# Performance work log

Hardware: AMD Instinct MI355X
Metric: run time of the kernel (lower is better)

## Reference

```python
import jax, jax.numpy as jnp
import numpy as np

E, C, N, W_IN, W_OUT = 5, 2, 2048, 512, 256


def setup_inputs() -> dict:
    key = jax.random.key(0)
    ks = jax.random.split(key, 11)
    A = jax.random.uniform(ks[0], (E, N, N), dtype=jnp.float32)  # stacked edge-type adjacencies
    X = jax.random.normal(ks[1], (N, W_IN), dtype=jnp.float32)
    # GTConv weights (out_channels=C, in_channels=E), init std=0.01 as in torch
    gt_w0a = 0.01 * jax.random.normal(ks[2], (C, E), dtype=jnp.float32)
    gt_w0b = 0.01 * jax.random.normal(ks[3], (C, E), dtype=jnp.float32)
    gt_w1 = 0.01 * jax.random.normal(ks[4], (C, E), dtype=jnp.float32)
    gcn_w = jax.random.normal(ks[5], (W_IN, W_OUT), dtype=jnp.float32) / np.sqrt(W_IN)
    gcn_b = jnp.zeros((W_OUT,), dtype=jnp.float32)
    lin1_w = 0.02 * jax.random.normal(ks[6], (W_OUT, C * W_OUT), dtype=jnp.float32)
    lin1_b = jnp.zeros((W_OUT,), dtype=jnp.float32)
    lin2_w = 0.02 * jax.random.normal(ks[7], (W_OUT, W_OUT), dtype=jnp.float32)
    lin2_b = jnp.zeros((W_OUT,), dtype=jnp.float32)
    return {"A": A, "X": X, "gt_w0a": gt_w0a, "gt_w0b": gt_w0b, "gt_w1": gt_w1,
            "gcn_w": gcn_w, "gcn_b": gcn_b, "lin1_w": lin1_w, "lin1_b": lin1_b,
            "lin2_w": lin2_w, "lin2_b": lin2_b}


def _gtconv(w, A):
    # softmax over edge types, weighted sum of adjacencies == coalesce of scaled edge lists
    f = jax.nn.softmax(w, axis=1)  # (C, E)
    return jnp.einsum('ce,enm->cnm', f, A)  # (C, N, N)


def _normalize(H):
    # remove self loops, then divide each entry by its column (target) degree
    n = H.shape[-1]
    H = H * (1.0 - jnp.eye(n, dtype=H.dtype))
    deg = H.sum(axis=-2)                      # (C, N) column sums == scatter_add over col
    safe = jnp.where(deg != 0, deg, 1.0)
    dinv = jnp.where(deg != 0, 1.0 / safe, 0.0)
    return H * dinv[:, None, :]


def reference(A, X, gt_w0a, gt_w0b, gt_w1, gcn_w, gcn_b, lin1_w, lin1_b, lin2_w, lin2_b):
    # layer 0 (first=True): two GTConvs, per-channel spspmm == batched matmul
    Ha = _gtconv(gt_w0a, A)
    Hb = _gtconv(gt_w0b, A)
    H = _normalize(jnp.einsum('cij,cjk->cik', Ha, Hb))
    # layer 1 (first=False): H_ @ conv1(A)
    Hb2 = _gtconv(gt_w1, A)
    H = _normalize(jnp.einsum('cij,cjk->cik', H, Hb2))
    # GCNConv per channel: add self loops, symmetric deg^{-1/2} normalization, aggregate to col
    n = H.shape[-1]
    M = H + jnp.eye(n, dtype=H.dtype)         # (C, N, N)
    deg = M.sum(axis=-2)                      # (C, N)
    safe = jnp.where(deg > 0, deg, 1.0)
    dis = jnp.where(deg > 0, safe ** -0.5, 0.0)
    Ahat = dis[:, :, None] * M * dis[:, None, :]
    XW = X @ gcn_w                            # (N, W_OUT)
    out = jnp.einsum('crn,rf->cnf', Ahat, XW) + gcn_b  # out[c,n] = sum_r Ahat[c,r,n] XW[r]
    out = jax.nn.relu(out)                    # (C, N, W_OUT)
    Xcat = out.transpose(1, 0, 2).reshape(n, -1)       # concat channels along dim=1
    h = jax.nn.relu(Xcat @ lin1_w.T + lin1_b)
    return h @ lin2_w.T + lin2_b
```

## Files before the change

kernel.cpp:

```cpp
#include <hip/hip_runtime.h>
#include <cstdint>
#include <cstddef>

#define NN   2048
#define N2   (2048LL*2048LL)
#define CC   2
#define EE   5
#define WIN  512
#define WOUT 256

typedef __bf16 bf16_t;
typedef __attribute__((ext_vector_type(8))) __bf16 bf16x8;
typedef __attribute__((ext_vector_type(4))) __bf16 bf16x4;
typedef __attribute__((ext_vector_type(4))) float  f32x4;

__global__ void k_prep(const float* __restrict__ X, const float* __restrict__ l1w,
                       const float* __restrict__ l2w, const float* __restrict__ gcnw,
                       bf16_t* __restrict__ Xb, bf16_t* __restrict__ l1wb,
                       bf16_t* __restrict__ l2wb, bf16_t* __restrict__ gwT) {
  __shared__ bf16_t tile[64][65];
  int bid = blockIdx.x;
  if (bid < 608) {
    int i = bid * 256 + threadIdx.x;
    const float* src; bf16_t* dst; int off;
    if (i < 131072)      { src = X;   dst = Xb;   off = i; }
    else if (i < 147456) { src = l1w; dst = l1wb; off = i - 131072; }
    else if (i < 155648) { src = l2w; dst = l2wb; off = i - 147456; }
    else return;
    float4 a = ((const float4*)src)[off * 2];
    float4 b = ((const float4*)src)[off * 2 + 1];
    bf16x8 o;
    o[0] = (bf16_t)a.x; o[1] = (bf16_t)a.y; o[2] = (bf16_t)a.z; o[3] = (bf16_t)a.w;
    o[4] = (bf16_t)b.x; o[5] = (bf16_t)b.y; o[6] = (bf16_t)b.z; o[7] = (bf16_t)b.w;
    ((bf16x8*)dst)[off] = o;
  } else {
    int b2 = bid - 608;
    int m0 = (b2 & 7) * 64, n0 = (b2 >> 3) * 64;
    int t = threadIdx.x, tr = t >> 4, tc = (t & 15) << 2;
#pragma unroll
    for (int v = 0; v < 4; ++v) {
      int r = tr + v * 16;
      float4 d = *(const float4*)&gcnw[(long long)(m0 + r) * WOUT + n0 + tc];
      tile[r][tc + 0] = (bf16_t)d.x; tile[r][tc + 1] = (bf16_t)d.y;
      tile[r][tc + 2] = (bf16_t)d.z; tile[r][tc + 3] = (bf16_t)d.w;
    }
    __syncthreads();
#pragma unroll
    for (int v = 0; v < 4; ++v) {
      int r = tr + v * 16;
      bf16x4 o;
      o[0] = tile[tc + 0][r]; o[1] = tile[tc + 1][r];
      o[2] = tile[tc + 2][r]; o[3] = tile[tc + 3][r];
      *(bf16x4*)&gwT[(long long)(n0 + r) * WIN + m0 + tc] = o;
    }
  }
}


__global__ void k_combine(const float* __restrict__ A,
                          const float* __restrict__ w0a, const float* __restrict__ w0b,
                          const float* __restrict__ w1,
                          bf16_t* __restrict__ Ha, bf16_t* __restrict__ HbT,
                          bf16_t* __restrict__ Hb2T, float* __restrict__ part) {
  __shared__ bf16_t tl[2][64][65];
  __shared__ float cs[2][16][64];
  float f[3][2][5];
  {
    const float* wp[3] = {w0a, w0b, w1};
#pragma unroll
    for (int w = 0; w < 3; ++w)
#pragma unroll
      for (int c = 0; c < 2; ++c) {
        float x[5], m = -1e30f, s = 0.f;
#pragma unroll
        for (int e = 0; e < 5; ++e) { x[e] = wp[w][c * 5 + e]; m = fmaxf(m, x[e]); }
#pragma unroll
        for (int e = 0; e < 5; ++e) { x[e] = expf(x[e] - m); s += x[e]; }
#pragma unroll
        for (int e = 0; e < 5; ++e) f[w][c][e] = x[e] / s;
      }
  }
  int i0 = blockIdx.x * 64, j0 = blockIdx.y * 64;
  int t = threadIdx.x, tr = t >> 4, tc = (t & 15) << 2;
  float cs0[4] = {0, 0, 0, 0}, cs1[4] = {0, 0, 0, 0};
  bf16x4 hb2a[4], hb2b[4];

#pragma unroll
  for (int v = 0; v < 4; ++v) {
    int lr = tr + v * 16;
    long long gi = i0 + lr;
    const float* base = A + gi * (long long)NN + j0 + tc;
    float av[5][4];
#pragma unroll
    for (int e = 0; e < 5; ++e) {
      float4 q = *(const float4*)(base + (long long)e * N2);
      av[e][0] = q.x; av[e][1] = q.y; av[e][2] = q.z; av[e][3] = q.w;
    }
    bf16x4 ha0, ha1;
#pragma unroll
    for (int x = 0; x < 4; ++x) {
      float s0 = 0.f, s1 = 0.f, s2 = 0.f, s3 = 0.f, s4 = 0.f, s5 = 0.f;
#pragma unroll
      for (int e = 0; e < 5; ++e) {
        float u = av[e][x];
        s0 += f[0][0][e] * u; s1 += f[0][1][e] * u;
        s2 += f[1][0][e] * u; s3 += f[1][1][e] * u;
        s4 += f[2][0][e] * u; s5 += f[2][1][e] * u;
      }
      ha0[x] = (bf16_t)s0; cs0[x] += (float)ha0[x];
      ha1[x] = (bf16_t)s1; cs1[x] += (float)ha1[x];
      tl[0][lr][tc + x] = (bf16_t)s2; tl[1][lr][tc + x] = (bf16_t)s3;
      hb2a[v][x] = (bf16_t)s4; hb2b[v][x] = (bf16_t)s5;
    }
    *(bf16x4*)&Ha[0 * N2 + gi * NN + j0 + tc] = ha0;
    *(bf16x4*)&Ha[1 * N2 + gi * NN + j0 + tc] = ha1;
  }
#pragma unroll
  for (int x = 0; x < 4; ++x) { cs[0][tr][tc + x] = cs0[x]; cs[1][tr][tc + x] = cs1[x]; }
  __syncthreads();

#pragma unroll
  for (int v = 0; v < 4; ++v) {
    int lr = tr + v * 16;
#pragma unroll
    for (int ch = 0; ch < 2; ++ch) {
      bf16x4 o;
      o[0] = tl[ch][tc + 0][lr]; o[1] = tl[ch][tc + 1][lr];
      o[2] = tl[ch][tc + 2][lr]; o[3] = tl[ch][tc + 3][lr];
      *(bf16x4*)&HbT[(long long)ch * N2 + (long long)(j0 + lr) * NN + i0 + tc] = o;
    }
  }
  if (t < 128) {
    int ch = t >> 6, col = t & 63;
    float s = 0.f;
#pragma unroll
    for (int r = 0; r < 16; ++r) s += cs[ch][r][col];
    part[((long long)ch * 32 + blockIdx.x) * NN + j0 + col] = s;
  }
  __syncthreads();

#pragma unroll
  for (int v = 0; v < 4; ++v) {
    int lr = tr + v * 16;
#pragma unroll
    for (int x = 0; x < 4; ++x) {
      tl[0][lr][tc + x] = hb2a[v][x];
      tl[1][lr][tc + x] = hb2b[v][x];
    }
  }
  __syncthreads();

#pragma unroll
  for (int v = 0; v < 4; ++v) {
    int lr = tr + v * 16;
#pragma unroll
    for (int ch = 0; ch < 2; ++ch) {
      bf16x4 o;
      o[0] = tl[ch][tc + 0][lr]; o[1] = tl[ch][tc + 1][lr];
      o[2] = tl[ch][tc + 2][lr]; o[3] = tl[ch][tc + 3][lr];
      *(bf16x4*)&Hb2T[(long long)ch * N2 + (long long)(j0 + lr) * NN + i0 + tc] = o;
    }
  }
}

__global__ void k_s_finish(const float* __restrict__ part, float* __restrict__ s) {
  int idx = blockIdx.x * 256 + threadIdx.x;
  int c = idx >> 11, k = idx & 2047;
  float acc = 0.f;
#pragma unroll
  for (int ib = 0; ib < 32; ++ib) acc += part[((long long)c * 32 + ib) * NN + k];
  s[idx] = acc;
}

template<bool EMIT_DIS>
__global__ void k_deg(const float* __restrict__ svec, const bf16_t* __restrict__ Arows,
                      const bf16_t* __restrict__ BT,
                      float* __restrict__ out1, float* __restrict__ out2,
                      float* __restrict__ out3) {
  int c = blockIdx.y;
  int j = blockIdx.x * 4 + (threadIdx.x >> 6);
  int lane = threadIdx.x & 63;
  const bf16_t* a = Arows + (long long)c * N2 + (long long)j * NN;
  const bf16_t* b = BT + (long long)c * N2 + (long long)j * NN;
  const float* s = svec + c * NN;
  float acc_s = 0.f, acc_a = 0.f;
#pragma unroll
  for (int it = 0; it < 4; ++it) {
    int k0 = (lane + it * 64) * 8;
    bf16x8 av = *(const bf16x8*)(a + k0);
    bf16x8 bv = *(const bf16x8*)(b + k0);
    float4 s0 = *(const float4*)(s + k0);
    float4 s1 = *(const float4*)(s + k0 + 4);
    float sv[8] = {s0.x, s0.y, s0.z, s0.w, s1.x, s1.y, s1.z, s1.w};
#pragma unroll
    for (int x = 0; x < 8; ++x) {
      float bx = (float)bv[x];
      acc_s += sv[x] * bx;
      acc_a += (float)av[x] * bx;
    }
  }
#pragma unroll
  for (int o = 32; o > 0; o >>= 1) {
    acc_s += __shfl_xor(acc_s, o, 64);
    acc_a += __shfl_xor(acc_a, o, 64);
  }
  if (lane == 0) {
    float deg = acc_s - acc_a;
    bool nz = (deg != 0.f);
    if (!EMIT_DIS) {
      out1[c * NN + j] = nz ? 1.f / deg : 0.f;
      out2[c * NN + j] = nz ? 1.f : 0.f;
    } else {
      float dis = nz ? 0.70710678118654752f : 1.f;
      out1[c * NN + j] = nz ? dis / deg : 0.f;
      out2[c * NN + j] = dis;
      out3[c * NN + j] = acc_a;
    }
  }
}

__global__ void k_scale_xwd(const bf16_t* __restrict__ XWT, const float* __restrict__ disv,
                            bf16_t* __restrict__ XWdT) {
  int i = blockIdx.x * 256 + threadIdx.x;
  int c = i >> 16, rem = i & 65535;
  bf16x8 v = ((const bf16x8*)XWT)[rem];
  int col0 = (rem & 255) * 8;
  float4 d0 = *(const float4*)(disv + c * NN + col0);
  float4 d1 = *(const float4*)(disv + c * NN + col0 + 4);
  bf16x8 o;
  o[0] = (bf16_t)((float)v[0] * d0.x); o[1] = (bf16_t)((float)v[1] * d0.y);
  o[2] = (bf16_t)((float)v[2] * d0.z); o[3] = (bf16_t)((float)v[3] * d0.w);
  o[4] = (bf16_t)((float)v[4] * d1.x); o[5] = (bf16_t)((float)v[5] * d1.y);
  o[6] = (bf16_t)((float)v[6] * d1.z); o[7] = (bf16_t)((float)v[7] * d1.w);
  ((bf16x8*)XWdT)[i] = o;
}


__global__ __launch_bounds__(256)
void k_gemmL(const bf16_t* __restrict__ A, const bf16_t* __restrict__ B,
             bf16_t* __restrict__ Hn, bf16_t* __restrict__ HnT,
             const float* __restrict__ dinv) {
  __shared__ __align__(16) char smem[65536];
  bf16_t* As = (bf16_t*)smem;
  bf16_t* Bs = (bf16_t*)(smem + 32768);
  bf16_t* tile = (bf16_t*)smem;

  int cz = blockIdx.z;
  const bf16_t* Ab = A + cz * N2 + (long long)blockIdx.x * 128 * NN;
  const bf16_t* Bb = B + cz * N2 + (long long)blockIdx.y * 128 * NN;

  int t = threadIdx.x, wid = t >> 6, lane = t & 63;
  int wr = wid >> 1, wc = wid & 1;
  f32x4 acc[4][4] = {};
  int frow = lane & 15;
  int fk_sw = (((lane >> 4) ^ ((frow >> 1) & 3)) << 3);
  int srow = t >> 2;
  int scol_sw = (((t & 3) ^ ((t >> 3) & 3)) << 3);

  auto STAGE = [&](int TT, int BUF) {
#pragma unroll
    for (int s = 0; s < 2; ++s) {
      long long kko = (long long)TT * 64 + s * 32 + scol_sw;
      const bf16_t* ga0 = Ab + (long long)srow * NN + kko;
      const bf16_t* gb0 = Bb + (long long)srow * NN + kko;
      char* la = smem + BUF * 16384 + s * 8192 + wid * 1024;
      char* lb = smem + 32768 + BUF * 16384 + s * 8192 + wid * 1024;
      __builtin_amdgcn_global_load_lds((__attribute__((address_space(1))) void*)ga0,
          (__attribute__((address_space(3))) void*)la, 16, 0, 0);
      __builtin_amdgcn_global_load_lds((__attribute__((address_space(1))) void*)(ga0 + 64LL * NN),
          (__attribute__((address_space(3))) void*)(la + 4096), 16, 0, 0);
      __builtin_amdgcn_global_load_lds((__attribute__((address_space(1))) void*)gb0,
          (__attribute__((address_space(3))) void*)lb, 16, 0, 0);
      __builtin_amdgcn_global_load_lds((__attribute__((address_space(1))) void*)(gb0 + 64LL * NN),
          (__attribute__((address_space(3))) void*)(lb + 4096), 16, 0, 0);
    }
  };
  auto COMPUTE = [&](int BUF) {
#pragma unroll
    for (int ks = 0; ks < 2; ++ks) {
      bf16x8 af[4], bfr[4];
#pragma unroll
      for (int m = 0; m < 4; ++m)
        af[m] = *(const bf16x8*)&As[BUF * 8192 + ks * 4096 + (wr * 64 + m * 16 + frow) * 32 + fk_sw];
#pragma unroll
      for (int n = 0; n < 4; ++n)
        bfr[n] = *(const bf16x8*)&Bs[BUF * 8192 + ks * 4096 + (wc * 64 + n * 16 + frow) * 32 + fk_sw];
      __builtin_amdgcn_s_setprio(1);
#pragma unroll
      for (int m = 0; m < 4; ++m)
#pragma unroll
        for (int n = 0; n < 4; ++n)
          acc[m][n] = __builtin_amdgcn_mfma_f32_16x16x32_bf16(af[m], bfr[n], acc[m][n], 0, 0, 0);
      __builtin_amdgcn_s_setprio(0);
    }
  };

  const int nt = 32;
  STAGE(0, 0); STAGE(1, 1);
  for (int tt = 0; tt < nt; ++tt) {
    if (tt < nt - 1) asm volatile("s_waitcnt vmcnt(8)" ::: "memory");
    else             asm volatile("s_waitcnt vmcnt(0)" ::: "memory");
    __builtin_amdgcn_s_barrier();
    __builtin_amdgcn_sched_barrier(0);
    COMPUTE(tt & 1);
    __builtin_amdgcn_s_barrier();
    if (tt + 2 < nt) STAGE(tt + 2, tt & 1);
  }
  __builtin_amdgcn_sched_barrier(0);

  int rl0 = wr * 64 + ((lane >> 4) << 2);
  int cl0 = wc * 64 + (lane & 15);
  int r0 = blockIdx.x * 128 + rl0;
  int c0 = blockIdx.y * 128 + cl0;

  bf16_t* Cb = Hn + cz * N2;
  bf16_t* Ct = HnT + cz * N2;
  float dj[4];
#pragma unroll
  for (int n = 0; n < 4; ++n) dj[n] = dinv[cz * NN + c0 + n * 16];
#pragma unroll
  for (int m = 0; m < 4; ++m)
#pragma unroll
    for (int n = 0; n < 4; ++n)
#pragma unroll
      for (int j = 0; j < 4; ++j) {
        int r = r0 + m * 16 + j, col = c0 + n * 16;
        float v = (r == col) ? 0.f : acc[m][n][j] * dj[n];
        Cb[(long long)r * NN + col] = (bf16_t)v;
        tile[(rl0 + m * 16 + j) * 130 + cl0 + n * 16] = (bf16_t)v;
      }
  __syncthreads();
  int nl = t >> 5, rl = (t & 31) * 4;
#pragma unroll
  for (int vv = 0; vv < 16; ++vv) {
    int n_l = nl + vv * 8;
    bf16x4 o;
    o[0] = tile[(rl + 0) * 130 + n_l]; o[1] = tile[(rl + 1) * 130 + n_l];
    o[2] = tile[(rl + 2) * 130 + n_l]; o[3] = tile[(rl + 3) * 130 + n_l];
    *(bf16x4*)&Ct[(long long)(blockIdx.y * 128 + n_l) * NN + blockIdx.x * 128 + rl] = o;
  }
}


enum { EP_F32 = 0, EP_BRELU = 3, EP_BF32 = 4, EP_XWT = 5, EP_BF16O = 7 };

template<int EP>
__global__ __launch_bounds__(256)
void k_gemm(const bf16_t* __restrict__ A, const bf16_t* __restrict__ B,
            void* __restrict__ Cv,
            const float* __restrict__ aux1, const float* __restrict__ aux2,
            bf16_t* __restrict__ aux3,
            int N, int K, int lda, int ldb,
            long long zA, long long zB, long long zC) {
  __shared__ __align__(16) char smem[36864];
  bf16_t* As = (bf16_t*)smem;
  bf16_t* Bs = (bf16_t*)(smem + 24576);
  bf16_t* tile = (bf16_t*)smem;

  int cz = blockIdx.z;
  const bf16_t* Ab = A + cz * zA + (long long)blockIdx.x * 128 * lda;
  const bf16_t* Bb = B + cz * zB + (long long)blockIdx.y * 64 * ldb;

  int t = threadIdx.x, wid = t >> 6, lane = t & 63;
  int wr = wid >> 1, wc = wid & 1;
  f32x4 acc[4][2] = {};
  int frow = lane & 15;
  int fk_sw = (((lane >> 4) ^ ((frow >> 1) & 3)) << 3);
  int srow = t >> 2;
  int scol_sw = (((t & 3) ^ ((t >> 3) & 3)) << 3);
  int nt = K >> 5;

  auto STAGE = [&](int TT, int BUF) {
    long long kko = (long long)TT * 32 + scol_sw;
    const bf16_t* ga0 = Ab + (long long)srow * lda + kko;
    const bf16_t* ga1 = Ab + (long long)(64 + srow) * lda + kko;
    const bf16_t* gb0 = Bb + (long long)srow * ldb + kko;
    char* la = smem + BUF * 8192 + wid * 1024;
    char* lb = smem + 24576 + BUF * 4096 + wid * 1024;
    __builtin_amdgcn_global_load_lds((__attribute__((address_space(1))) void*)ga0,
        (__attribute__((address_space(3))) void*)la, 16, 0, 0);
    __builtin_amdgcn_global_load_lds((__attribute__((address_space(1))) void*)ga1,
        (__attribute__((address_space(3))) void*)(la + 4096), 16, 0, 0);
    __builtin_amdgcn_global_load_lds((__attribute__((address_space(1))) void*)gb0,
        (__attribute__((address_space(3))) void*)lb, 16, 0, 0);
  };
  auto COMPUTE = [&](int BUF) {
    bf16x8 af[4], bfr[2];
#pragma unroll
    for (int m = 0; m < 4; ++m)
      af[m] = *(const bf16x8*)&As[BUF * 4096 + (wr * 64 + m * 16 + frow) * 32 + fk_sw];
#pragma unroll
    for (int n = 0; n < 2; ++n)
      bfr[n] = *(const bf16x8*)&Bs[BUF * 2048 + (wc * 32 + n * 16 + frow) * 32 + fk_sw];
#pragma unroll
    for (int m = 0; m < 4; ++m)
#pragma unroll
      for (int n = 0; n < 2; ++n)
        acc[m][n] = __builtin_amdgcn_mfma_f32_16x16x32_bf16(af[m], bfr[n], acc[m][n], 0, 0, 0);
  };

  STAGE(0, 0); STAGE(1, 1); STAGE(2, 2);
  int slot = 0;
  for (int tt = 0; tt < nt; ++tt) {
    int rem = nt - 1 - tt;
    if (rem >= 2)      asm volatile("s_waitcnt vmcnt(6)" ::: "memory");
    else if (rem == 1) asm volatile("s_waitcnt vmcnt(3)" ::: "memory");
    else               asm volatile("s_waitcnt vmcnt(0)" ::: "memory");
    __builtin_amdgcn_s_barrier();
    __builtin_amdgcn_sched_barrier(0);
    COMPUTE(slot);
    __builtin_amdgcn_s_barrier();
    if (tt + 3 < nt) STAGE(tt + 3, slot);
    slot = (slot == 2) ? 0 : slot + 1;
  }
  __builtin_amdgcn_sched_barrier(0);

  int rl0 = wr * 64 + ((lane >> 4) << 2);
  int cl0 = wc * 32 + (lane & 15);
  int r0 = blockIdx.x * 128 + rl0;
  int c0 = blockIdx.y * 64 + cl0;

  if constexpr (EP == EP_F32) {
    float* Cb = (float*)Cv + cz * zC;
#pragma unroll
    for (int m = 0; m < 4; ++m)
#pragma unroll
      for (int n = 0; n < 2; ++n)
#pragma unroll
        for (int j = 0; j < 4; ++j)
          Cb[(long long)(r0 + m * 16 + j) * N + c0 + n * 16] = acc[m][n][j];
  } else if constexpr (EP == EP_BF16O) {
    bf16_t* Cb = (bf16_t*)Cv + cz * zC;
#pragma unroll
    for (int m = 0; m < 4; ++m)
#pragma unroll
      for (int n = 0; n < 2; ++n)
#pragma unroll
        for (int j = 0; j < 4; ++j)
          Cb[(long long)(r0 + m * 16 + j) * N + c0 + n * 16] = (bf16_t)acc[m][n][j];
  } else if constexpr (EP == EP_XWT) {
    float* Cb = (float*)Cv;
#pragma unroll
    for (int m = 0; m < 4; ++m)
#pragma unroll
      for (int n = 0; n < 2; ++n)
#pragma unroll
        for (int j = 0; j < 4; ++j) {
          float v = acc[m][n][j];
          Cb[(long long)(r0 + m * 16 + j) * N + c0 + n * 16] = v;
          tile[(rl0 + m * 16 + j) * 65 + cl0 + n * 16] = (bf16_t)v;
        }
    __syncthreads();
    int nl = t >> 5, rl = (t & 31) * 4;
#pragma unroll
    for (int vv = 0; vv < 8; ++vv) {
      int n_l = nl + vv * 8;
      bf16x4 o;
      o[0] = tile[(rl + 0) * 65 + n_l]; o[1] = tile[(rl + 1) * 65 + n_l];
      o[2] = tile[(rl + 2) * 65 + n_l]; o[3] = tile[(rl + 3) * 65 + n_l];
      *(bf16x4*)&aux3[(long long)(blockIdx.y * 64 + n_l) * NN + blockIdx.x * 128 + rl] = o;
    }
  } else if constexpr (EP == EP_BRELU) {
    bf16_t* Cb = (bf16_t*)Cv;
    float bj[2];
#pragma unroll
    for (int n = 0; n < 2; ++n) bj[n] = aux1[c0 + n * 16];
#pragma unroll
    for (int m = 0; m < 4; ++m)
#pragma unroll
      for (int n = 0; n < 2; ++n)
#pragma unroll
        for (int j = 0; j < 4; ++j)
          Cb[(long long)(r0 + m * 16 + j) * N + c0 + n * 16] =
              (bf16_t)fmaxf(acc[m][n][j] + bj[n], 0.f);
  } else {
    float* Cb = (float*)Cv;
    float bj[2];
#pragma unroll
    for (int n = 0; n < 2; ++n) bj[n] = aux1[c0 + n * 16];
#pragma unroll
    for (int m = 0; m < 4; ++m)
#pragma unroll
      for (int n = 0; n < 2; ++n)
#pragma unroll
        for (int j = 0; j < 4; ++j)
          Cb[(long long)(r0 + m * 16 + j) * N + c0 + n * 16] = acc[m][n][j] + bj[n];
  }
}


__global__ void k_gcn_epi2(const float* __restrict__ Z, const float* __restrict__ XW,
                           const float* __restrict__ gcn_b, const float* __restrict__ cscal,
                           const float* __restrict__ disv, const float* __restrict__ Mdiag,
                           bf16_t* __restrict__ Xcat) {
  long long idx4 = ((long long)blockIdx.x * 256 + threadIdx.x) * 4;
  int c = (int)(idx4 >> 19);
  int rem = (int)(idx4 & ((1 << 19) - 1));
  int n = rem >> 8, fcol = rem & 255;
  float4 z  = *(const float4*)(Z + (long long)c * NN * WOUT + rem);
  float4 xw = *(const float4*)(XW + rem);
  float4 b  = *(const float4*)(gcn_b + fcol);
  float cs = cscal[c * NN + n], dn = disv[c * NN + n], md = Mdiag[c * NN + n];
  float d2 = dn * dn, mdd = md * dn;
  bf16x4 o;
  o[0] = (bf16_t)fmaxf(cs * (z.x - mdd * xw.x) + d2 * xw.x + b.x, 0.f);
  o[1] = (bf16_t)fmaxf(cs * (z.y - mdd * xw.y) + d2 * xw.y + b.y, 0.f);
  o[2] = (bf16_t)fmaxf(cs * (z.z - mdd * xw.z) + d2 * xw.z + b.z, 0.f);
  o[3] = (bf16_t)fmaxf(cs * (z.w - mdd * xw.w) + d2 * xw.w + b.w, 0.f);
  *(bf16x4*)&Xcat[(long long)n * (CC * WOUT) + c * WOUT + fcol] = o;
}


extern "C" void kernel_launch(void* const* d_in, const int* in_sizes, int n_in,
                              void* d_out, int out_size, void* d_ws, size_t ws_size,
                              hipStream_t stream) {
  const float* A    = (const float*)d_in[0];
  const float* X    = (const float*)d_in[1];
  const float* w0a  = (const float*)d_in[2];
  const float* w0b  = (const float*)d_in[3];
  const float* w1   = (const float*)d_in[4];
  const float* gcnw = (const float*)d_in[5];
  const float* gcnb = (const float*)d_in[6];
  const float* l1w  = (const float*)d_in[7];
  const float* l1b  = (const float*)d_in[8];
  const float* l2w  = (const float*)d_in[9];
  const float* l2b  = (const float*)d_in[10];
  float* out = (float*)d_out;

  char* p = (char*)d_ws;
  auto carve = [&](size_t bytes) -> char* {
    char* r = p; p += (bytes + 255) & ~(size_t)255; return r;
  };
  float*  svec  = (float*)carve((size_t)CC * NN * 4);
  float*  dinv1 = (float*)carve((size_t)CC * NN * 4);
  float*  m1    = (float*)carve((size_t)CC * NN * 4);
  float*  cscal = (float*)carve((size_t)CC * NN * 4);
  float*  disv  = (float*)carve((size_t)CC * NN * 4);
  float*  Mdiag = (float*)carve((size_t)CC * NN * 4);
  float*  part  = (float*)carve((size_t)CC * 32 * NN * 4);
  bf16_t* S1    = (bf16_t*)carve((size_t)CC * N2 * 2);
  bf16_t* HbT   = (bf16_t*)carve((size_t)CC * N2 * 2);
  bf16_t* Hb2T  = (bf16_t*)carve((size_t)CC * N2 * 2);
  bf16_t* Hn    = (bf16_t*)carve((size_t)CC * N2 * 2);
  bf16_t* HnT   = (bf16_t*)carve((size_t)CC * N2 * 2);
  bf16_t* Xb    = (bf16_t*)carve((size_t)NN * WIN * 2);
  bf16_t* gwT   = (bf16_t*)carve((size_t)WOUT * WIN * 2);
  bf16_t* l1wb  = (bf16_t*)carve((size_t)WOUT * CC * WOUT * 2);
  bf16_t* l2wb  = (bf16_t*)carve((size_t)WOUT * WOUT * 2);
  float*  XW    = (float*)carve((size_t)NN * WOUT * 4);
  bf16_t* XWT   = (bf16_t*)carve((size_t)WOUT * NN * 2);
  bf16_t* Xcat  = (bf16_t*)carve((size_t)NN * CC * WOUT * 2);
  bf16_t* hb    = (bf16_t*)carve((size_t)NN * WOUT * 2);

  bf16_t* Ha = S1;
  bf16_t* XWdT = (bf16_t*)((char*)S1);
  bf16_t* Yt   = (bf16_t*)((char*)S1 + (2LL << 20));
  float*  Z    = (float*) ((char*)S1 + (6LL << 20));

  k_prep<<<640, 256, 0, stream>>>(X, l1w, l2w, gcnw, Xb, l1wb, l2wb, gwT);
  k_combine<<<dim3(32, 32), 256, 0, stream>>>(A, w0a, w0b, w1, Ha, HbT, Hb2T, part);
  k_s_finish<<<16, 256, 0, stream>>>(part, svec);

  k_deg<false><<<dim3(512, 2), 256, 0, stream>>>(svec, Ha, HbT, dinv1, m1, nullptr);
  k_gemmL<<<dim3(16, 16, 2), 256, 0, stream>>>(Ha, HbT, Hn, HnT, dinv1);

  k_deg<true><<<dim3(512, 2), 256, 0, stream>>>(m1, Hn, Hb2T, cscal, disv, Mdiag);

  k_gemm<EP_XWT><<<dim3(16, 4, 1), 256, 0, stream>>>(
      Xb, gwT, XW, nullptr, nullptr, XWT, WOUT, WIN, WIN, WIN, 0, 0, 0);
  k_scale_xwd<<<512, 256, 0, stream>>>(XWT, disv, XWdT);
  k_gemm<EP_BF16O><<<dim3(2, 32, 2), 256, 0, stream>>>(
      XWdT, HnT, Yt, nullptr, nullptr, nullptr, NN, NN, NN, NN,
      (long long)WOUT * NN, N2, (long long)WOUT * NN);
  k_gemm<EP_F32><<<dim3(16, 4, 2), 256, 0, stream>>>(
      Hb2T, Yt, Z, nullptr, nullptr, nullptr, WOUT, NN, NN, NN,
      N2, (long long)WOUT * NN, (long long)NN * WOUT);
  k_gcn_epi2<<<1024, 256, 0, stream>>>(Z, XW, gcnb, cscal, disv, Mdiag, Xcat);

  k_gemm<EP_BRELU><<<dim3(16, 4, 1), 256, 0, stream>>>(
      Xcat, l1wb, hb, l1b, nullptr, nullptr, WOUT, CC * WOUT, CC * WOUT, CC * WOUT, 0, 0, 0);
  k_gemm<EP_BF32><<<dim3(16, 4, 1), 256, 0, stream>>>(
      hb, l2wb, out, l2b, nullptr, nullptr, WOUT, WOUT, WOUT, WOUT, 0, 0, 0);
}
```

Before: 149.9 us.

## Fuse prep, scaling and GCN epilogue kernels into neighbouring launches

Merges the weight/X bf16 conversion into the combine kernel as extra blocks, folds the dis-scaling of XW^T into the XW GEMM epilogue, and folds the GCN epilogue into the Z GEMM so Z is never materialized in fp32. The combine column-sum reduction now uses wave shuffles instead of a 16-row shared array. This removes three launches and the round trips through the XWT and Z buffers, at the cost of more complex epilogues with uncoalesced scalar stores and gathers in the GCN epilogue.

```diff
diff --git a/kernel.cpp b/kernel.cpp
--- a/kernel.cpp
+++ b/kernel.cpp
@@ -14,56 +14,63 @@
 typedef __attribute__((ext_vector_type(4))) __bf16 bf16x4;
 typedef __attribute__((ext_vector_type(4))) float  f32x4;
 
-__global__ void k_prep(const float* __restrict__ X, const float* __restrict__ l1w,
-                       const float* __restrict__ l2w, const float* __restrict__ gcnw,
-                       bf16_t* __restrict__ Xb, bf16_t* __restrict__ l1wb,
-                       bf16_t* __restrict__ l2wb, bf16_t* __restrict__ gwT) {
-  __shared__ bf16_t tile[64][65];
-  int bid = blockIdx.x;
-  if (bid < 608) {
-    int i = bid * 256 + threadIdx.x;
-    const float* src; bf16_t* dst; int off;
-    if (i < 131072)      { src = X;   dst = Xb;   off = i; }
-    else if (i < 147456) { src = l1w; dst = l1wb; off = i - 131072; }
-    else if (i < 155648) { src = l2w; dst = l2wb; off = i - 147456; }
-    else return;
-    float4 a = ((const float4*)src)[off * 2];
-    float4 b = ((const float4*)src)[off * 2 + 1];
-    bf16x8 o;
-    o[0] = (bf16_t)a.x; o[1] = (bf16_t)a.y; o[2] = (bf16_t)a.z; o[3] = (bf16_t)a.w;
-    o[4] = (bf16_t)b.x; o[5] = (bf16_t)b.y; o[6] = (bf16_t)b.z; o[7] = (bf16_t)b.w;
-    ((bf16x8*)dst)[off] = o;
-  } else {
-    int b2 = bid - 608;
-    int m0 = (b2 & 7) * 64, n0 = (b2 >> 3) * 64;
-    int t = threadIdx.x, tr = t >> 4, tc = (t & 15) << 2;
-#pragma unroll
-    for (int v = 0; v < 4; ++v) {
-      int r = tr + v * 16;
-      float4 d = *(const float4*)&gcnw[(long long)(m0 + r) * WOUT + n0 + tc];
-      tile[r][tc + 0] = (bf16_t)d.x; tile[r][tc + 1] = (bf16_t)d.y;
-      tile[r][tc + 2] = (bf16_t)d.z; tile[r][tc + 3] = (bf16_t)d.w;
-    }
-    __syncthreads();
-#pragma unroll
-    for (int v = 0; v < 4; ++v) {
-      int r = tr + v * 16;
-      bf16x4 o;
-      o[0] = tile[tc + 0][r]; o[1] = tile[tc + 1][r];
-      o[2] = tile[tc + 2][r]; o[3] = tile[tc + 3][r];
-      *(bf16x4*)&gwT[(long long)(n0 + r) * WIN + m0 + tc] = o;
-    }
-  }
-}
+#define AS1 __attribute__((address_space(1)))
+#define AS3 __attribute__((address_space(3)))
 
 
 __global__ void k_combine(const float* __restrict__ A,
                           const float* __restrict__ w0a, const float* __restrict__ w0b,
                           const float* __restrict__ w1,
                           bf16_t* __restrict__ Ha, bf16_t* __restrict__ HbT,
-                          bf16_t* __restrict__ Hb2T, float* __restrict__ part) {
+                          bf16_t* __restrict__ Hb2T, float* __restrict__ part,
+                          const float* __restrict__ X, const float* __restrict__ l1w,
+                          const float* __restrict__ l2w, const float* __restrict__ gcnw,
+                          bf16_t* __restrict__ Xb, bf16_t* __restrict__ l1wb,
+                          bf16_t* __restrict__ l2wb, bf16_t* __restrict__ gwT) {
   __shared__ bf16_t tl[2][64][65];
-  __shared__ float cs[2][16][64];
+  __shared__ float cs[2][4][64];
+  int bid = blockIdx.x;
+  int t = threadIdx.x;
+
+  if (bid >= 1024) {
+    int bid2 = bid - 1024;
+    if (bid2 < 608) {
+      int i = bid2 * 256 + t;
+      const float* src; bf16_t* dst; int off;
+      if (i < 131072)      { src = X;   dst = Xb;   off = i; }
+      else if (i < 147456) { src = l1w; dst = l1wb; off = i - 131072; }
+      else                 { src = l2w; dst = l2wb; off = i - 147456; }
+      float4 a = ((const float4*)src)[off * 2];
+      float4 b = ((const float4*)src)[off * 2 + 1];
+      bf16x8 o;
+      o[0] = (bf16_t)a.x; o[1] = (bf16_t)a.y; o[2] = (bf16_t)a.z; o[3] = (bf16_t)a.w;
+      o[4] = (bf16_t)b.x; o[5] = (bf16_t)b.y; o[6] = (bf16_t)b.z; o[7] = (bf16_t)b.w;
+      ((bf16x8*)dst)[off] = o;
+    } else {
+      int b2 = bid2 - 608;
+      int m0 = (b2 & 7) * 64, n0 = (b2 >> 3) * 64;
+      int tr = t >> 4, tc = (t & 15) << 2;
+      bf16_t (*tile)[65] = (bf16_t (*)[65])&tl[0][0][0];
+#pragma unroll
+      for (int v = 0; v < 4; ++v) {
+        int r = tr + v * 16;
+        float4 d = *(const float4*)&gcnw[(long long)(m0 + r) * WOUT + n0 + tc];
+        tile[r][tc + 0] = (bf16_t)d.x; tile[r][tc + 1] = (bf16_t)d.y;
+        tile[r][tc + 2] = (bf16_t)d.z; tile[r][tc + 3] = (bf16_t)d.w;
+      }
+      __syncthreads();
+#pragma unroll
+      for (int v = 0; v < 4; ++v) {
+        int r = tr + v * 16;
+        bf16x4 o;
+        o[0] = tile[tc + 0][r]; o[1] = tile[tc + 1][r];
+        o[2] = tile[tc + 2][r]; o[3] = tile[tc + 3][r];
+        *(bf16x4*)&gwT[(long long)(n0 + r) * WIN + m0 + tc] = o;
+      }
+    }
+    return;
+  }
+
   float f[3][2][5];
   {
     const float* wp[3] = {w0a, w0b, w1};
@@ -80,8 +87,9 @@
         for (int e = 0; e < 5; ++e) f[w][c][e] = x[e] / s;
       }
   }
-  int i0 = blockIdx.x * 64, j0 = blockIdx.y * 64;
-  int t = threadIdx.x, tr = t >> 4, tc = (t & 15) << 2;
+  int i0 = (bid >> 5) * 64, j0 = (bid & 31) * 64;
+  int tr = t >> 4, tc = (t & 15) << 2;
+  int lane = t & 63, wid = t >> 6;
   float cs0[4] = {0, 0, 0, 0}, cs1[4] = {0, 0, 0, 0};
   bf16x4 hb2a[4], hb2b[4];
 
@@ -116,7 +124,15 @@
     *(bf16x4*)&Ha[1 * N2 + gi * NN + j0 + tc] = ha1;
   }
 #pragma unroll
-  for (int x = 0; x < 4; ++x) { cs[0][tr][tc + x] = cs0[x]; cs[1][tr][tc + x] = cs1[x]; }
+  for (int x = 0; x < 4; ++x) {
+    float a0 = cs0[x], a1 = cs1[x];
+    a0 += __shfl_xor(a0, 16, 64); a0 += __shfl_xor(a0, 32, 64);
+    a1 += __shfl_xor(a1, 16, 64); a1 += __shfl_xor(a1, 32, 64);
+    if ((lane >> 4) == 0) {
+      cs[0][wid][(lane & 15) * 4 + x] = a0;
+      cs[1][wid][(lane & 15) * 4 + x] = a1;
+    }
+  }
   __syncthreads();
 
 #pragma unroll
@@ -132,10 +148,8 @@
   }
   if (t < 128) {
     int ch = t >> 6, col = t & 63;
-    float s = 0.f;
-#pragma unroll
-    for (int r = 0; r < 16; ++r) s += cs[ch][r][col];
-    part[((long long)ch * 32 + blockIdx.x) * NN + j0 + col] = s;
+    float s = cs[ch][0][col] + cs[ch][1][col] + cs[ch][2][col] + cs[ch][3][col];
+    part[((long long)ch * 32 + (bid >> 5)) * NN + j0 + col] = s;
   }
   __syncthreads();
 
@@ -219,22 +233,6 @@
   }
 }
 
-__global__ void k_scale_xwd(const bf16_t* __restrict__ XWT, const float* __restrict__ disv,
-                            bf16_t* __restrict__ XWdT) {
-  int i = blockIdx.x * 256 + threadIdx.x;
-  int c = i >> 16, rem = i & 65535;
-  bf16x8 v = ((const bf16x8*)XWT)[rem];
-  int col0 = (rem & 255) * 8;
-  float4 d0 = *(const float4*)(disv + c * NN + col0);
-  float4 d1 = *(const float4*)(disv + c * NN + col0 + 4);
-  bf16x8 o;
-  o[0] = (bf16_t)((float)v[0] * d0.x); o[1] = (bf16_t)((float)v[1] * d0.y);
-  o[2] = (bf16_t)((float)v[2] * d0.z); o[3] = (bf16_t)((float)v[3] * d0.w);
-  o[4] = (bf16_t)((float)v[4] * d1.x); o[5] = (bf16_t)((float)v[5] * d1.y);
-  o[6] = (bf16_t)((float)v[6] * d1.z); o[7] = (bf16_t)((float)v[7] * d1.w);
-  ((bf16x8*)XWdT)[i] = o;
-}
-
 
 __global__ __launch_bounds__(256)
 void k_gemmL(const bf16_t* __restrict__ A, const bf16_t* __restrict__ B,
@@ -265,14 +263,10 @@
       const bf16_t* gb0 = Bb + (long long)srow * NN + kko;
       char* la = smem + BUF * 16384 + s * 8192 + wid * 1024;
       char* lb = smem + 32768 + BUF * 16384 + s * 8192 + wid * 1024;
-      __builtin_amdgcn_global_load_lds((__attribute__((address_space(1))) void*)ga0,
-          (__attribute__((address_space(3))) void*)la, 16, 0, 0);
-      __builtin_amdgcn_global_load_lds((__attribute__((address_space(1))) void*)(ga0 + 64LL * NN),
-          (__attribute__((address_space(3))) void*)(la + 4096), 16, 0, 0);
-      __builtin_amdgcn_global_load_lds((__attribute__((address_space(1))) void*)gb0,
-          (__attribute__((address_space(3))) void*)lb, 16, 0, 0);
-      __builtin_amdgcn_global_load_lds((__attribute__((address_space(1))) void*)(gb0 + 64LL * NN),
-          (__attribute__((address_space(3))) void*)(lb + 4096), 16, 0, 0);
+      __builtin_amdgcn_global_load_lds((AS1 void*)ga0, (AS3 void*)la, 16, 0, 0);
+      __builtin_amdgcn_global_load_lds((AS1 void*)(ga0 + 64LL * NN), (AS3 void*)(la + 4096), 16, 0, 0);
+      __builtin_amdgcn_global_load_lds((AS1 void*)gb0, (AS3 void*)lb, 16, 0, 0);
+      __builtin_amdgcn_global_load_lds((AS1 void*)(gb0 + 64LL * NN), (AS3 void*)(lb + 4096), 16, 0, 0);
     }
   };
   auto COMPUTE = [&](int BUF) {
@@ -342,14 +336,14 @@
 }
 
 
-enum { EP_F32 = 0, EP_BRELU = 3, EP_BF32 = 4, EP_XWT = 5, EP_BF16O = 7 };
+enum { EP_BRELU = 3, EP_BF32 = 4, EP_BF16O = 7, EP_XWDT = 8, EP_GCN = 9 };
 
 template<int EP>
 __global__ __launch_bounds__(256)
 void k_gemm(const bf16_t* __restrict__ A, const bf16_t* __restrict__ B,
             void* __restrict__ Cv,
             const float* __restrict__ aux1, const float* __restrict__ aux2,
-            bf16_t* __restrict__ aux3,
+            bf16_t* __restrict__ aux3, const float* __restrict__ aux4,
             int N, int K, int lda, int ldb,
             long long zA, long long zB, long long zC) {
   __shared__ __align__(16) char smem[36864];
@@ -377,12 +371,9 @@
     const bf16_t* gb0 = Bb + (long long)srow * ldb + kko;
     char* la = smem + BUF * 8192 + wid * 1024;
     char* lb = smem + 24576 + BUF * 4096 + wid * 1024;
-    __builtin_amdgcn_global_load_lds((__attribute__((address_space(1))) void*)ga0,
-        (__attribute__((address_space(3))) void*)la, 16, 0, 0);
-    __builtin_amdgcn_global_load_lds((__attribute__((address_space(1))) void*)ga1,
-        (__attribute__((address_space(3))) void*)(la + 4096), 16, 0, 0);
-    __builtin_amdgcn_global_load_lds((__attribute__((address_space(1))) void*)gb0,
-        (__attribute__((address_space(3))) void*)lb, 16, 0, 0);
+    __builtin_amdgcn_global_load_lds((AS1 void*)ga0, (AS3 void*)la, 16, 0, 0);
+    __builtin_amdgcn_global_load_lds((AS1 void*)ga1, (AS3 void*)(la + 4096), 16, 0, 0);
+    __builtin_amdgcn_global_load_lds((AS1 void*)gb0, (AS3 void*)lb, 16, 0, 0);
   };
   auto COMPUTE = [&](int BUF) {
     bf16x8 af[4], bfr[2];
@@ -420,16 +411,7 @@
   int r0 = blockIdx.x * 128 + rl0;
   int c0 = blockIdx.y * 64 + cl0;
 
-  if constexpr (EP == EP_F32) {
-    float* Cb = (float*)Cv + cz * zC;
-#pragma unroll
-    for (int m = 0; m < 4; ++m)
-#pragma unroll
-      for (int n = 0; n < 2; ++n)
-#pragma unroll
-        for (int j = 0; j < 4; ++j)
-          Cb[(long long)(r0 + m * 16 + j) * N + c0 + n * 16] = acc[m][n][j];
-  } else if constexpr (EP == EP_BF16O) {
+  if constexpr (EP == EP_BF16O) {
     bf16_t* Cb = (bf16_t*)Cv + cz * zC;
 #pragma unroll
     for (int m = 0; m < 4; ++m)
@@ -438,7 +420,7 @@
 #pragma unroll
         for (int j = 0; j < 4; ++j)
           Cb[(long long)(r0 + m * 16 + j) * N + c0 + n * 16] = (bf16_t)acc[m][n][j];
-  } else if constexpr (EP == EP_XWT) {
+  } else if constexpr (EP == EP_XWDT) {
     float* Cb = (float*)Cv;
 #pragma unroll
     for (int m = 0; m < 4; ++m)
@@ -455,11 +437,43 @@
 #pragma unroll
     for (int vv = 0; vv < 8; ++vv) {
       int n_l = nl + vv * 8;
-      bf16x4 o;
-      o[0] = tile[(rl + 0) * 65 + n_l]; o[1] = tile[(rl + 1) * 65 + n_l];
-      o[2] = tile[(rl + 2) * 65 + n_l]; o[3] = tile[(rl + 3) * 65 + n_l];
-      *(bf16x4*)&aux3[(long long)(blockIdx.y * 64 + n_l) * NN + blockIdx.x * 128 + rl] = o;
-    }
+      bf16x4 v4;
+      v4[0] = tile[(rl + 0) * 65 + n_l]; v4[1] = tile[(rl + 1) * 65 + n_l];
+      v4[2] = tile[(rl + 2) * 65 + n_l]; v4[3] = tile[(rl + 3) * 65 + n_l];
+      int i0 = blockIdx.x * 128 + rl;
+      long long row = (long long)(blockIdx.y * 64 + n_l) * NN + i0;
+#pragma unroll
+      for (int c = 0; c < 2; ++c) {
+        float4 dv = *(const float4*)&aux2[c * NN + i0];
+        bf16x4 o;
+        o[0] = (bf16_t)((float)v4[0] * dv.x); o[1] = (bf16_t)((float)v4[1] * dv.y);
+        o[2] = (bf16_t)((float)v4[2] * dv.z); o[3] = (bf16_t)((float)v4[3] * dv.w);
+        *(bf16x4*)&aux3[(long long)c * WOUT * NN + row] = o;
+      }
+    }
+  } else if constexpr (EP == EP_GCN) {
+    bf16_t* Cb = (bf16_t*)Cv;
+    const float* XWp = aux1;
+    const float* csp = aux2 + cz * NN;
+    const float* dnp = aux2 + CC * NN + cz * NN;
+    const float* mdp = aux2 + 2 * CC * NN + cz * NN;
+    float bj[2];
+#pragma unroll
+    for (int n = 0; n < 2; ++n) bj[n] = aux4[c0 + n * 16];
+#pragma unroll
+    for (int m = 0; m < 4; ++m)
+#pragma unroll
+      for (int j = 0; j < 4; ++j) {
+        int r = r0 + m * 16 + j;
+        float csv = csp[r], dnv = dnp[r], mdv = mdp[r];
+        float mdd = mdv * dnv, d2 = dnv * dnv;
+#pragma unroll
+        for (int n = 0; n < 2; ++n) {
+          float xw = XWp[(long long)r * WOUT + c0 + n * 16];
+          float v = fmaxf(csv * (acc[m][n][j] - mdd * xw) + d2 * xw + bj[n], 0.f);
+          Cb[(long long)r * (CC * WOUT) + cz * WOUT + c0 + n * 16] = (bf16_t)v;
+        }
+      }
   } else if constexpr (EP == EP_BRELU) {
     bf16_t* Cb = (bf16_t*)Cv;
     float bj[2];
@@ -486,28 +500,6 @@
         for (int j = 0; j < 4; ++j)
           Cb[(long long)(r0 + m * 16 + j) * N + c0 + n * 16] = acc[m][n][j] + bj[n];
   }
-}
-
-
-__global__ void k_gcn_epi2(const float* __restrict__ Z, const float* __restrict__ XW,
-                           const float* __restrict__ gcn_b, const float* __restrict__ cscal,
-                           const float* __restrict__ disv, const float* __restrict__ Mdiag,
-                           bf16_t* __restrict__ Xcat) {
-  long long idx4 = ((long long)blockIdx.x * 256 + threadIdx.x) * 4;
-  int c = (int)(idx4 >> 19);
-  int rem = (int)(idx4 & ((1 << 19) - 1));
-  int n = rem >> 8, fcol = rem & 255;
-  float4 z  = *(const float4*)(Z + (long long)c * NN * WOUT + rem);
-  float4 xw = *(const float4*)(XW + rem);
-  float4 b  = *(const float4*)(gcn_b + fcol);
-  float cs = cscal[c * NN + n], dn = disv[c * NN + n], md = Mdiag[c * NN + n];
-  float d2 = dn * dn, mdd = md * dn;
-  bf16x4 o;
-  o[0] = (bf16_t)fmaxf(cs * (z.x - mdd * xw.x) + d2 * xw.x + b.x, 0.f);
-  o[1] = (bf16_t)fmaxf(cs * (z.y - mdd * xw.y) + d2 * xw.y + b.y, 0.f);
-  o[2] = (bf16_t)fmaxf(cs * (z.z - mdd * xw.z) + d2 * xw.z + b.z, 0.f);
-  o[3] = (bf16_t)fmaxf(cs * (z.w - mdd * xw.w) + d2 * xw.w + b.w, 0.f);
-  *(bf16x4*)&Xcat[(long long)n * (CC * WOUT) + c * WOUT + fcol] = o;
 }
 
 
@@ -534,9 +526,7 @@
   float*  svec  = (float*)carve((size_t)CC * NN * 4);
   float*  dinv1 = (float*)carve((size_t)CC * NN * 4);
   float*  m1    = (float*)carve((size_t)CC * NN * 4);
-  float*  cscal = (float*)carve((size_t)CC * NN * 4);
-  float*  disv  = (float*)carve((size_t)CC * NN * 4);
-  float*  Mdiag = (float*)carve((size_t)CC * NN * 4);
+  float*  scal  = (float*)carve((size_t)3 * CC * NN * 4);
   float*  part  = (float*)carve((size_t)CC * 32 * NN * 4);
   bf16_t* S1    = (bf16_t*)carve((size_t)CC * N2 * 2);
   bf16_t* HbT   = (bf16_t*)carve((size_t)CC * N2 * 2);
@@ -548,37 +538,35 @@
   bf16_t* l1wb  = (bf16_t*)carve((size_t)WOUT * CC * WOUT * 2);
   bf16_t* l2wb  = (bf16_t*)carve((size_t)WOUT * WOUT * 2);
   float*  XW    = (float*)carve((size_t)NN * WOUT * 4);
-  bf16_t* XWT   = (bf16_t*)carve((size_t)WOUT * NN * 2);
   bf16_t* Xcat  = (bf16_t*)carve((size_t)NN * CC * WOUT * 2);
   bf16_t* hb    = (bf16_t*)carve((size_t)NN * WOUT * 2);
 
   bf16_t* Ha = S1;
   bf16_t* XWdT = (bf16_t*)((char*)S1);
   bf16_t* Yt   = (bf16_t*)((char*)S1 + (2LL << 20));
-  float*  Z    = (float*) ((char*)S1 + (6LL << 20));
-
-  k_prep<<<640, 256, 0, stream>>>(X, l1w, l2w, gcnw, Xb, l1wb, l2wb, gwT);
-  k_combine<<<dim3(32, 32), 256, 0, stream>>>(A, w0a, w0b, w1, Ha, HbT, Hb2T, part);
+  float*  disv = scal + CC * NN;
+
+  k_combine<<<1664, 256, 0, stream>>>(A, w0a, w0b, w1, Ha, HbT, Hb2T, part,
+                                      X, l1w, l2w, gcnw, Xb, l1wb, l2wb, gwT);
   k_s_finish<<<16, 256, 0, stream>>>(part, svec);
 
   k_deg<false><<<dim3(512, 2), 256, 0, stream>>>(svec, Ha, HbT, dinv1, m1, nullptr);
   k_gemmL<<<dim3(16, 16, 2), 256, 0, stream>>>(Ha, HbT, Hn, HnT, dinv1);
 
-  k_deg<true><<<dim3(512, 2), 256, 0, stream>>>(m1, Hn, Hb2T, cscal, disv, Mdiag);
-
-  k_gemm<EP_XWT><<<dim3(16, 4, 1), 256, 0, stream>>>(
-      Xb, gwT, XW, nullptr, nullptr, XWT, WOUT, WIN, WIN, WIN, 0, 0, 0);
-  k_scale_xwd<<<512, 256, 0, stream>>>(XWT, disv, XWdT);
+  k_deg<true><<<dim3(512, 2), 256, 0, stream>>>(m1, Hn, Hb2T,
+                                                scal, scal + CC * NN, scal + 2 * CC * NN);
+
+  k_gemm<EP_XWDT><<<dim3(16, 4, 1), 256, 0, stream>>>(
+      Xb, gwT, XW, nullptr, disv, XWdT, nullptr, WOUT, WIN, WIN, WIN, 0, 0, 0);
   k_gemm<EP_BF16O><<<dim3(2, 32, 2), 256, 0, stream>>>(
-      XWdT, HnT, Yt, nullptr, nullptr, nullptr, NN, NN, NN, NN,
+      XWdT, HnT, Yt, nullptr, nullptr, nullptr, nullptr, NN, NN, NN, NN,
       (long long)WOUT * NN, N2, (long long)WOUT * NN);
-  k_gemm<EP_F32><<<dim3(16, 4, 2), 256, 0, stream>>>(
-      Hb2T, Yt, Z, nullptr, nullptr, nullptr, WOUT, NN, NN, NN,
-      N2, (long long)WOUT * NN, (long long)NN * WOUT);
-  k_gcn_epi2<<<1024, 256, 0, stream>>>(Z, XW, gcnb, cscal, disv, Mdiag, Xcat);
+  k_gemm<EP_GCN><<<dim3(16, 4, 2), 256, 0, stream>>>(
+      Hb2T, Yt, Xcat, XW, scal, nullptr, gcnb, WOUT, NN, NN, NN,
+      N2, (long long)WOUT * NN, 0);
 
   k_gemm<EP_BRELU><<<dim3(16, 4, 1), 256, 0, stream>>>(
-      Xcat, l1wb, hb, l1b, nullptr, nullptr, WOUT, CC * WOUT, CC * WOUT, CC * WOUT, 0, 0, 0);
+      Xcat, l1wb, hb, l1b, nullptr, nullptr, nullptr, WOUT, CC * WOUT, CC * WOUT, CC * WOUT, 0, 0, 0);
   k_gemm<EP_BF32><<<dim3(16, 4, 1), 256, 0, stream>>>(
-      hb, l2wb, out, l2b, nullptr, nullptr, WOUT, WOUT, WOUT, WOUT, 0, 0, 0);
+      hb, l2wb, out, l2b, nullptr, nullptr, nullptr, WOUT, WOUT, WOUT, WOUT, 0, 0, 0);
 }
```

Result: faster. 144.1 us (median of 2 runs) (-3.9%).
